# Optimization experiments

Hardware: AMD Instinct MI355X
Metric: run time of the kernel (lower is better)

Reference implementation:

```python
import jax, jax.numpy as jnp
import numpy as np

B, S, D, H = 2, 2048, 1024, 16
DK = D // H  # 64
THETA = 10000.0


def _rope_tables(seq_len, d_k, theta):
    pos = jnp.arange(seq_len, dtype=jnp.float32)  # [S]
    dim = jnp.arange(0, d_k, 2, dtype=jnp.float32)  # [DK/2]
    inv_freq = 1.0 / theta ** (dim / d_k)
    angle = pos[:, None] * inv_freq[None, :]  # [S, DK/2]
    angle = jnp.repeat(angle, 2, axis=-1)  # repeat_interleave -> [S, DK]
    return jnp.cos(angle), jnp.sin(angle)


def _apply_rope(x, cos, sin):
    # x: [..., S, DK]; interleaved pair rotation
    x1 = x[..., ::2]
    x2 = x[..., 1::2]
    x_perm = jnp.stack([-x2, x1], axis=-1).reshape(x.shape)
    return x * cos + x_perm * sin


def setup_inputs() -> dict:
    key = jax.random.key(0)
    ks = jax.random.split(key, 5)
    std = np.sqrt(2.0 / (D + D)).astype(np.float32)
    return {
        "x": jax.random.normal(ks[0], (B, S, D), dtype=jnp.float32),
        "Wq": jax.random.normal(ks[1], (D, D), dtype=jnp.float32) * std,
        "Wk": jax.random.normal(ks[2], (D, D), dtype=jnp.float32) * std,
        "Wv": jax.random.normal(ks[3], (D, D), dtype=jnp.float32) * std,
        "Wo": jax.random.normal(ks[4], (D, D), dtype=jnp.float32) * std,
    }


def reference(x, Wq, Wk, Wv, Wo):
    seq_len = x.shape[-2]
    # projections: weight is [d_out, d_in], applied as x @ W^T
    def split_heads(t):
        return t.reshape(*t.shape[:-1], H, DK).swapaxes(-3, -2)  # [B, H, S, DK]

    Q = split_heads(jnp.einsum('bsd,od->bso', x, Wq))
    K = split_heads(jnp.einsum('bsd,od->bso', x, Wk))
    V = split_heads(jnp.einsum('bsd,od->bso', x, Wv))

    cos, sin = _rope_tables(seq_len, DK, THETA)  # [S, DK]
    Q = _apply_rope(Q, cos, sin)
    K = _apply_rope(K, cos, sin)

    scale = 1.0 / np.sqrt(DK).astype(np.float32)
    logits = jnp.einsum('bhnd,bhmd->bhnm', Q, K) * scale  # [B, H, S, S]
    causal = jnp.tril(jnp.ones((seq_len, seq_len), dtype=bool))
    logits = jnp.where(causal, logits, -jnp.inf)
    probs = jax.nn.softmax(logits, axis=-1)
    attn = jnp.einsum('bhnm,bhmd->bhnd', probs, V)  # [B, H, S, DK]
    attn = attn.swapaxes(-3, -2).reshape(*x.shape[:-1], D)  # [B, S, D]
    return jnp.einsum('bsd,od->bso', attn, Wo)
```

## Files before the change

### kernel.cpp

```cpp
#include <hip/hip_runtime.h>
#include <hip/hip_bf16.h>
#include <cstdint>
#include <cstddef>

#define BB 2
#define SS 2048
#define DD 1024
#define HH 16
#define DKK 64
#define MM (BB*SS)

typedef __bf16 bf16x8 __attribute__((ext_vector_type(8)));
typedef float  f32x4  __attribute__((ext_vector_type(4)));

__device__ __forceinline__ unsigned short f2bf(float f) {
    unsigned u = __float_as_uint(f);
    u += 0x7FFF + ((u >> 16) & 1);
    return (unsigned short)(u >> 16);
}

#if __has_builtin(__builtin_amdgcn_cvt_pk_bf16_f32)
typedef __bf16 bf16v2 __attribute__((ext_vector_type(2)));
__device__ __forceinline__ unsigned pk_bf16(float a, float b) {
    bf16v2 v = __builtin_amdgcn_cvt_pk_bf16_f32(a, b);
    return __builtin_bit_cast(unsigned, v);
}
#else
__device__ __forceinline__ unsigned pk_bf16(float a, float b) {
    return (unsigned)f2bf(a) | ((unsigned)f2bf(b) << 16);
}
#endif

__device__ __forceinline__ void gld_lds16(const void* g, void* l) {
    __builtin_amdgcn_global_load_lds(
        (const __attribute__((address_space(1))) unsigned int*)g,
        (__attribute__((address_space(3))) unsigned int*)l, 16, 0, 0);
}

#define WAIT_VM8() __builtin_amdgcn_s_waitcnt(0x0F78)
#define WAIT_VM4() __builtin_amdgcn_s_waitcnt(0x0F74)
#define WAIT_VM3() __builtin_amdgcn_s_waitcnt(0x0F73)
#define WAIT_VM0() __builtin_amdgcn_s_waitcnt(0x0F70)
#define BARRIER()  __builtin_amdgcn_s_barrier()

__global__ __launch_bounds__(256) void cast_all(const float* __restrict__ x,
                                                const float* __restrict__ wq,
                                                const float* __restrict__ wk,
                                                const float* __restrict__ wv,
                                                const float* __restrict__ wo,
                                                unsigned short* __restrict__ xb,
                                                unsigned short* __restrict__ wb) {
    int i = (blockIdx.x * 256 + threadIdx.x) * 4;
    const float* src;
    unsigned short* dst;
    if (i < MM * DD) { src = x + i; dst = xb + i; }
    else {
        int e = i - MM * DD;
        int r = e >> 20;
        const float* s0 = (r == 0) ? wq : (r == 1) ? wk : (r == 2) ? wv : wo;
        src = s0 + (e & ((1 << 20) - 1));
        dst = wb + e;
    }
    float4 v = *reinterpret_cast<const float4*>(src);
    ushort4 o;
    o.x = f2bf(v.x); o.y = f2bf(v.y); o.z = f2bf(v.z); o.w = f2bf(v.w);
    *reinterpret_cast<ushort4*>(dst) = o;
}

__global__ __launch_bounds__(256, 3) void gemm_qkv(const unsigned short* __restrict__ A,
                                                   const unsigned short* __restrict__ W,
                                                   unsigned short* __restrict__ Qo,
                                                   unsigned short* __restrict__ Ko,
                                                   unsigned short* __restrict__ Vto) {
    __shared__ __align__(16) unsigned short A0[128 * 32], W0[128 * 32];
    __shared__ __align__(16) unsigned short A1[128 * 32], W1[128 * 32];
    const int tid  = threadIdx.x;
    const int wave = tid >> 6, lane = tid & 63;
    const int quad = lane >> 4, l16 = lane & 15;
    const int wm = wave >> 1, wn = wave & 1;
    const int m0 = blockIdx.y * 128, n0 = blockIdx.x * 128;
    const int sw3 = l16 & 3;

    f32x4 acc[4][4];
    for (int i = 0; i < 4; i++)
        for (int j = 0; j < 4; j++) acc[i][j] = f32x4{0.f, 0.f, 0.f, 0.f};

    auto stage = [&](int k0, unsigned short* As, unsigned short* Ws) {
        for (int c = tid; c < 512; c += 256) {
            int row = c >> 2, g = c & 3;
            int gc = ((g ^ (row & 3)) << 3);
            gld_lds16(A + (size_t)(m0 + row) * DD + k0 + gc, As + c * 8);
            gld_lds16(W + (size_t)(n0 + row) * DD + k0 + gc, Ws + c * 8);
        }
    };
    auto compute = [&](const unsigned short* As, const unsigned short* Ws) {
        bf16x8 af[4], bfb[4];
        for (int i = 0; i < 4; i++)
            af[i] = *reinterpret_cast<const bf16x8*>(As + (wm * 64 + i * 16 + l16) * 32 + ((quad ^ sw3) << 3));
        for (int j = 0; j < 4; j++)
            bfb[j] = *reinterpret_cast<const bf16x8*>(Ws + (wn * 64 + j * 16 + l16) * 32 + ((quad ^ sw3) << 3));
        for (int i = 0; i < 4; i++)
            for (int j = 0; j < 4; j++)
                acc[i][j] = __builtin_amdgcn_mfma_f32_16x16x32_bf16(af[i], bfb[j], acc[i][j], 0, 0, 0);
    };

    stage(0, A0, W0);
    int k0 = 0;
    while (true) {
        BARRIER();
        if (k0 + 32 < DD) { stage(k0 + 32, A1, W1); WAIT_VM4(); } else WAIT_VM0();
        BARRIER();
        compute(A0, W0);
        k0 += 32; if (k0 >= DD) break;

        BARRIER();
        if (k0 + 32 < DD) { stage(k0 + 32, A0, W0); WAIT_VM4(); } else WAIT_VM0();
        BARRIER();
        compute(A1, W1);
        k0 += 32; if (k0 >= DD) break;
    }

    const int region = n0 >> 10;
    const float L2T_OVER_DK = 13.287712379549449f / 64.0f;
    if (region < 2) {
        unsigned short* Co = region ? Ko : Qo;
        const float osc = (region == 0) ? 0.18033688011112042f : 1.0f;
        for (int i = 0; i < 4; i++) {
            int mrow = m0 + wm * 64 + i * 16 + quad * 4;
            int b = mrow >> 11, s0 = mrow & 2047;
            for (int j = 0; j < 4; j++) {
                int nc = (n0 + wn * 64 + j * 16 + l16) & 1023;
                int h = nc >> 6, dk = nc & 63;
                float inv_freq = exp2f(-(float)(dk & ~1) * L2T_OVER_DK);
                for (int r = 0; r < 4; r++) {
                    float v = acc[i][j][r];
                    float partner = __shfl_xor(v, 1, 64);
                    float sn, cs;
                    __sincosf((float)(s0 + r) * inv_freq, &sn, &cs);
                    float outv = (v * cs + ((dk & 1) ? partner : -partner) * sn) * osc;
                    Co[((size_t)(b * HH + h) * SS + (s0 + r)) * DKK + dk] = f2bf(outv);
                }
            }
        }
    } else {
        __syncthreads();
        unsigned short* T = A0 + wave * 1024;
        const int dkl = lane >> 2, s4 = (lane & 3) * 4;
        for (int i = 0; i < 4; i++) {
            int ms0 = m0 + wm * 64 + i * 16;
            for (int j = 0; j < 4; j++) {
                int nc0 = n0 + wn * 64 + j * 16;
                for (int r = 0; r < 4; r++)
                    T[(quad * 4 + r) * 17 + l16] = f2bf(acc[i][j][r]);
                ushort4 o;
                o.x = T[(s4 + 0) * 17 + dkl];
                o.y = T[(s4 + 1) * 17 + dkl];
                o.z = T[(s4 + 2) * 17 + dkl];
                o.w = T[(s4 + 3) * 17 + dkl];
                int nc = (nc0 + dkl) & 1023;
                int h = nc >> 6, dk = nc & 63;
                int m = ms0 + s4;
                int b = m >> 11, s = m & 2047;
                *reinterpret_cast<ushort4*>(Vto + ((size_t)((b * HH + h) * DKK + dk)) * SS + s) = o;
            }
        }
    }
}

__global__ __launch_bounds__(256, 3) void gemm_out(const unsigned short* __restrict__ A,
                                                   const unsigned short* __restrict__ W,
                                                   float* __restrict__ C) {
    __shared__ __align__(16) unsigned short A0[64 * 32], W0[128 * 32];
    __shared__ __align__(16) unsigned short A1[64 * 32], W1[128 * 32];
    const int tid  = threadIdx.x;
    const int wave = tid >> 6, lane = tid & 63;
    const int quad = lane >> 4, l16 = lane & 15;
    const int wm = wave >> 1, wn = wave & 1;
    const int m0 = blockIdx.y * 64, n0 = blockIdx.x * 128;
    const int sw3 = l16 & 3;

    f32x4 acc[2][4];
    for (int i = 0; i < 2; i++)
        for (int j = 0; j < 4; j++) acc[i][j] = f32x4{0.f, 0.f, 0.f, 0.f};

    auto stage = [&](int k0, unsigned short* As, unsigned short* Ws) {
        {
            int row = tid >> 2, g = tid & 3;
            int gc = ((g ^ (row & 3)) << 3);
            gld_lds16(A + (size_t)(m0 + row) * DD + k0 + gc, As + tid * 8);
        }
        for (int c = tid; c < 512; c += 256) {
            int row = c >> 2, g = c & 3;
            int gc = ((g ^ (row & 3)) << 3);
            gld_lds16(W + (size_t)(n0 + row) * DD + k0 + gc, Ws + c * 8);
        }
    };
    auto compute = [&](const unsigned short* As, const unsigned short* Ws) {
        bf16x8 af[2], bfb[4];
        for (int i = 0; i < 2; i++)
            af[i] = *reinterpret_cast<const bf16x8*>(As + (wm * 32 + i * 16 + l16) * 32 + ((quad ^ sw3) << 3));
        for (int j = 0; j < 4; j++)
            bfb[j] = *reinterpret_cast<const bf16x8*>(Ws + (wn * 64 + j * 16 + l16) * 32 + ((quad ^ sw3) << 3));
        for (int i = 0; i < 2; i++)
            for (int j = 0; j < 4; j++)
                acc[i][j] = __builtin_amdgcn_mfma_f32_16x16x32_bf16(af[i], bfb[j], acc[i][j], 0, 0, 0);
    };

    stage(0, A0, W0);
    int k0 = 0;
    while (true) {
        BARRIER();
        if (k0 + 32 < DD) { stage(k0 + 32, A1, W1); WAIT_VM3(); } else WAIT_VM0();
        BARRIER();
        compute(A0, W0);
        k0 += 32; if (k0 >= DD) break;

        BARRIER();
        if (k0 + 32 < DD) { stage(k0 + 32, A0, W0); WAIT_VM3(); } else WAIT_VM0();
        BARRIER();
        compute(A1, W1);
        k0 += 32; if (k0 >= DD) break;
    }

    for (int i = 0; i < 2; i++) {
        int mrow = m0 + wm * 32 + i * 16 + quad * 4;
        for (int j = 0; j < 4; j++) {
            int ncol = n0 + wn * 64 + j * 16 + l16;
            for (int r = 0; r < 4; r++)
                C[(size_t)(mrow + r) * DD + ncol] = acc[i][j][r];
        }
    }
}

__global__ __launch_bounds__(256, 3) void attn_kernel(const unsigned short* __restrict__ Qb,
                                                      const unsigned short* __restrict__ Kb,
                                                      const unsigned short* __restrict__ Vtb,
                                                      unsigned short* __restrict__ attn) {
    __shared__ unsigned short K0s[64 * 64], V0s[64 * 64];
    __shared__ unsigned short K1s[64 * 64], V1s[64 * 64];
    __shared__ unsigned short Ps[4][16 * 72];

    const int tid  = threadIdx.x;
    const int wave = tid >> 6, lane = tid & 63;
    const int quad = lane >> 4, l16 = lane & 15;

    const int lin = blockIdx.x;
    const int xcd = lin & 7, idx = lin >> 3;
    const int bh  = xcd * 4 + (idx & 3);
    const int tau = 31 - (idx >> 2);
    const int nST = tau + 1;

    const int swK = l16 & 7;
    const int q0r = tau * 64;

    const unsigned short* Qg = Qb  + (size_t)bh * SS * DKK;
    const unsigned short* Kg = Kb  + (size_t)bh * SS * DKK;
    const unsigned short* Vg = Vtb + (size_t)bh * DKK * SS;

    bf16x8 q0 = *reinterpret_cast<const bf16x8*>(Qg + (size_t)(q0r + wave * 16 + l16) * DKK + quad * 8);
    bf16x8 q1 = *reinterpret_cast<const bf16x8*>(Qg + (size_t)(q0r + wave * 16 + l16) * DKK + 32 + quad * 8);

    bf16x8 vone;
    for (int tt = 0; tt < 8; tt++) vone[tt] = (__bf16)1.0f;

    f32x4 ao[4], al;
    for (int j = 0; j < 4; j++) ao[j] = f32x4{0.f,0.f,0.f,0.f};
    al = f32x4{0.f,0.f,0.f,0.f};

    auto stage = [&](int s, unsigned short* Kd, unsigned short* Vd) {
        const int kv0 = s * 64;
        for (int c = tid; c < 512; c += 256) {
            int rowK = c >> 3, gK = c & 7;
            gld_lds16(Kg + (size_t)(kv0 + rowK) * DKK + ((gK ^ (rowK & 7)) << 3), Kd + c * 8);
            int rowV = c >> 3, gV = c & 7;
            gld_lds16(Vg + (size_t)rowV * SS + kv0 + ((gV ^ (rowV & 7)) << 3), Vd + c * 8);
        }
    };

    auto do_tile = [&](const unsigned short* Kd, const unsigned short* Vd, bool diag) {
        f32x4 sc[4];
        __builtin_amdgcn_s_setprio(1);
        for (int j = 0; j < 4; j++) {
            const unsigned short* kr = Kd + (j * 16 + l16) * 64;
            bf16x8 kf0 = *reinterpret_cast<const bf16x8*>(kr + ((quad ^ swK) << 3));
            bf16x8 kf1 = *reinterpret_cast<const bf16x8*>(kr + (((4 + quad) ^ swK) << 3));
            f32x4 s = f32x4{0.f, 0.f, 0.f, 0.f};
            s = __builtin_amdgcn_mfma_f32_16x16x32_bf16(q0, kf0, s, 0, 0, 0);
            s = __builtin_amdgcn_mfma_f32_16x16x32_bf16(q1, kf1, s, 0, 0, 0);
            sc[j] = s;
        }
        __builtin_amdgcn_s_setprio(0);
        if (diag) {
            for (int j = 0; j < 4; j++) {
                int lcol = j * 16 + l16;
                for (int r = 0; r < 4; r++) {
                    int lrow = wave * 16 + quad * 4 + r;
                    if (lcol > lrow) sc[j][r] = -1e30f;
                }
            }
        }
        for (int j = 0; j < 4; j++)
            for (int r = 0; r < 4; r++)
                sc[j][r] = exp2f(sc[j][r]);

        unsigned short* Pw = Ps[wave];
        for (int r = 0; r < 4; r++) {
            unsigned pA = pk_bf16(sc[0][r], sc[1][r]);
            unsigned pB = pk_bf16(sc[2][r], sc[3][r]);
            int ro = (quad * 4 + r) * 72;
            Pw[ro + l16]      = (unsigned short)pA;
            Pw[ro + 16 + l16] = (unsigned short)(pA >> 16);
            Pw[ro + 32 + l16] = (unsigned short)pB;
            Pw[ro + 48 + l16] = (unsigned short)(pB >> 16);
        }

        __builtin_amdgcn_s_setprio(1);
        for (int ko = 0; ko < 64; ko += 32) {
            bf16x8 pf = *reinterpret_cast<const bf16x8*>(Pw + l16 * 72 + ko + quad * 8);
            al = __builtin_amdgcn_mfma_f32_16x16x32_bf16(pf, vone, al, 0, 0, 0);
            int gg = (ko >> 3) + quad;
            for (int j = 0; j < 4; j++) {
                bf16x8 vf = *reinterpret_cast<const bf16x8*>(Vd + (j * 16 + l16) * 64 + ((gg ^ (l16 & 7)) << 3));
                ao[j] = __builtin_amdgcn_mfma_f32_16x16x32_bf16(pf, vf, ao[j], 0, 0, 0);
            }
        }
        __builtin_amdgcn_s_setprio(0);
    };

    stage(0, K0s, V0s);
    int s = 0;
    while (true) {
        BARRIER();
        if (s + 1 < nST) { stage(s + 1, K1s, V1s); WAIT_VM4(); } else WAIT_VM0();
        BARRIER();
        do_tile(K0s, V0s, s == tau);
        if (++s >= nST) break;

        BARRIER();
        if (s + 1 < nST) { stage(s + 1, K0s, V0s); WAIT_VM4(); } else WAIT_VM0();
        BARRIER();
        do_tile(K1s, V1s, s == tau);
        if (++s >= nST) break;
    }

    const int b = bh >> 4, h = bh & 15;
    for (int r = 0; r < 4; r++) {
        float invL = __builtin_amdgcn_rcpf(al[r]);
        int sr = q0r + wave * 16 + quad * 4 + r;
        for (int j = 0; j < 4; j++)
            attn[((size_t)(b * SS + sr)) * DD + h * DKK + j * 16 + l16] = f2bf(ao[j][r] * invL);
    }
}

extern "C" void kernel_launch(void* const* d_in, const int* in_sizes, int n_in,
                              void* d_out, int out_size, void* d_ws, size_t ws_size,
                              hipStream_t stream) {
    const float* x  = (const float*)d_in[0];
    const float* Wq = (const float*)d_in[1];
    const float* Wk = (const float*)d_in[2];
    const float* Wv = (const float*)d_in[3];
    const float* Wo = (const float*)d_in[4];

    char* ws = (char*)d_ws;
    const size_t MB = 1u << 20;
    unsigned short* xb    = (unsigned short*)(ws);
    unsigned short* wb    = (unsigned short*)(ws + 8  * MB);
    unsigned short* Qbuf  = (unsigned short*)(ws + 16 * MB);
    unsigned short* Kbuf  = (unsigned short*)(ws + 24 * MB);
    unsigned short* Vtbuf = (unsigned short*)(ws + 32 * MB);
    unsigned short* attnb = xb;

    cast_all<<<8192, 256, 0, stream>>>(x, Wq, Wk, Wv, Wo, xb, wb);

    gemm_qkv<<<dim3(24, 32), 256, 0, stream>>>(xb, wb, Qbuf, Kbuf, Vtbuf);

    attn_kernel<<<dim3(1024), 256, 0, stream>>>(Qbuf, Kbuf, Vtbuf, attnb);

    gemm_out<<<dim3(8, 64), 256, 0, stream>>>(attnb, wb + 3 * 1024 * 1024, (float*)d_out);
}
```

Measured before the change: 178.7 us.

## Double query rows per attention block to reuse K/V tiles across 32-row wave groups

Each attention block now covers 128 query rows (32 per wave, as two 16-row groups) instead of 64, so every K/V tile staged in shared memory feeds twice as many MFMAs. The grid shrinks to 512 blocks, diagonal tiles carry a column offset for the causal mask, and tiles lying entirely above a wave's rows are skipped. The setprio hints are also dropped. In exchange, per-wave register and LDS use rises, there are fewer blocks to balance the causal triangle, and waves in a block can have uneven work on diagonal tiles.

```diff
diff --git a/kernel.cpp b/kernel.cpp
--- a/kernel.cpp
+++ b/kernel.cpp
@@ -238,7 +238,7 @@
                                                       unsigned short* __restrict__ attn) {
     __shared__ unsigned short K0s[64 * 64], V0s[64 * 64];
     __shared__ unsigned short K1s[64 * 64], V1s[64 * 64];
-    __shared__ unsigned short Ps[4][16 * 72];
+    __shared__ unsigned short Ps[4][32 * 72];
 
     const int tid  = threadIdx.x;
     const int wave = tid >> 6, lane = tid & 63;
@@ -247,25 +247,31 @@
     const int lin = blockIdx.x;
     const int xcd = lin & 7, idx = lin >> 3;
     const int bh  = xcd * 4 + (idx & 3);
-    const int tau = 31 - (idx >> 2);
-    const int nST = tau + 1;
+    const int tau = 15 - (idx >> 2);
+    const int nST = 2 * tau + 2;
 
     const int swK = l16 & 7;
-    const int q0r = tau * 64;
+    const int q0r = tau * 128;
+    const int wq0 = wave * 32;
 
     const unsigned short* Qg = Qb  + (size_t)bh * SS * DKK;
     const unsigned short* Kg = Kb  + (size_t)bh * SS * DKK;
     const unsigned short* Vg = Vtb + (size_t)bh * DKK * SS;
 
-    bf16x8 q0 = *reinterpret_cast<const bf16x8*>(Qg + (size_t)(q0r + wave * 16 + l16) * DKK + quad * 8);
-    bf16x8 q1 = *reinterpret_cast<const bf16x8*>(Qg + (size_t)(q0r + wave * 16 + l16) * DKK + 32 + quad * 8);
+    bf16x8 qf[2][2];
+    for (int g = 0; g < 2; g++)
+        for (int h = 0; h < 2; h++)
+            qf[g][h] = *reinterpret_cast<const bf16x8*>(
+                Qg + (size_t)(q0r + wq0 + g * 16 + l16) * DKK + h * 32 + quad * 8);
 
     bf16x8 vone;
     for (int tt = 0; tt < 8; tt++) vone[tt] = (__bf16)1.0f;
 
-    f32x4 ao[4], al;
-    for (int j = 0; j < 4; j++) ao[j] = f32x4{0.f,0.f,0.f,0.f};
-    al = f32x4{0.f,0.f,0.f,0.f};
+    f32x4 ao[2][4], al[2];
+    for (int g = 0; g < 2; g++) {
+        for (int j = 0; j < 4; j++) ao[g][j] = f32x4{0.f,0.f,0.f,0.f};
+        al[g] = f32x4{0.f,0.f,0.f,0.f};
+    }
 
     auto stage = [&](int s, unsigned short* Kd, unsigned short* Vd) {
         const int kv0 = s * 64;
@@ -277,54 +283,67 @@
         }
     };
 
-    auto do_tile = [&](const unsigned short* Kd, const unsigned short* Vd, bool diag) {
-        f32x4 sc[4];
-        __builtin_amdgcn_s_setprio(1);
+    auto do_tile = [&](const unsigned short* Kd, const unsigned short* Vd,
+                       bool diag, int doff) {
+        f32x4 sc[2][4];
         for (int j = 0; j < 4; j++) {
             const unsigned short* kr = Kd + (j * 16 + l16) * 64;
             bf16x8 kf0 = *reinterpret_cast<const bf16x8*>(kr + ((quad ^ swK) << 3));
             bf16x8 kf1 = *reinterpret_cast<const bf16x8*>(kr + (((4 + quad) ^ swK) << 3));
-            f32x4 s = f32x4{0.f, 0.f, 0.f, 0.f};
-            s = __builtin_amdgcn_mfma_f32_16x16x32_bf16(q0, kf0, s, 0, 0, 0);
-            s = __builtin_amdgcn_mfma_f32_16x16x32_bf16(q1, kf1, s, 0, 0, 0);
-            sc[j] = s;
-        }
-        __builtin_amdgcn_s_setprio(0);
+            for (int g = 0; g < 2; g++) {
+                f32x4 s = f32x4{0.f, 0.f, 0.f, 0.f};
+                s = __builtin_amdgcn_mfma_f32_16x16x32_bf16(qf[g][0], kf0, s, 0, 0, 0);
+                s = __builtin_amdgcn_mfma_f32_16x16x32_bf16(qf[g][1], kf1, s, 0, 0, 0);
+                sc[g][j] = s;
+            }
+        }
         if (diag) {
-            for (int j = 0; j < 4; j++) {
-                int lcol = j * 16 + l16;
-                for (int r = 0; r < 4; r++) {
-                    int lrow = wave * 16 + quad * 4 + r;
-                    if (lcol > lrow) sc[j][r] = -1e30f;
+            for (int g = 0; g < 2; g++)
+                for (int j = 0; j < 4; j++) {
+                    int lcol = doff + j * 16 + l16;
+                    for (int r = 0; r < 4; r++) {
+                        int lrow = wq0 + g * 16 + quad * 4 + r;
+                        if (lcol > lrow) sc[g][j][r] = -1e30f;
+                    }
                 }
-            }
-        }
-        for (int j = 0; j < 4; j++)
-            for (int r = 0; r < 4; r++)
-                sc[j][r] = exp2f(sc[j][r]);
+        }
+        for (int g = 0; g < 2; g++)
+            for (int j = 0; j < 4; j++)
+                for (int r = 0; r < 4; r++)
+                    sc[g][j][r] = exp2f(sc[g][j][r]);
 
         unsigned short* Pw = Ps[wave];
-        for (int r = 0; r < 4; r++) {
-            unsigned pA = pk_bf16(sc[0][r], sc[1][r]);
-            unsigned pB = pk_bf16(sc[2][r], sc[3][r]);
-            int ro = (quad * 4 + r) * 72;
-            Pw[ro + l16]      = (unsigned short)pA;
-            Pw[ro + 16 + l16] = (unsigned short)(pA >> 16);
-            Pw[ro + 32 + l16] = (unsigned short)pB;
-            Pw[ro + 48 + l16] = (unsigned short)(pB >> 16);
-        }
-
-        __builtin_amdgcn_s_setprio(1);
+        for (int g = 0; g < 2; g++)
+            for (int r = 0; r < 4; r++) {
+                unsigned pA = pk_bf16(sc[g][0][r], sc[g][1][r]);
+                unsigned pB = pk_bf16(sc[g][2][r], sc[g][3][r]);
+                int ro = (g * 16 + quad * 4 + r) * 72;
+                Pw[ro + l16]      = (unsigned short)pA;
+                Pw[ro + 16 + l16] = (unsigned short)(pA >> 16);
+                Pw[ro + 32 + l16] = (unsigned short)pB;
+                Pw[ro + 48 + l16] = (unsigned short)(pB >> 16);
+            }
+
         for (int ko = 0; ko < 64; ko += 32) {
-            bf16x8 pf = *reinterpret_cast<const bf16x8*>(Pw + l16 * 72 + ko + quad * 8);
-            al = __builtin_amdgcn_mfma_f32_16x16x32_bf16(pf, vone, al, 0, 0, 0);
+            bf16x8 pf[2];
+            for (int g = 0; g < 2; g++) {
+                pf[g] = *reinterpret_cast<const bf16x8*>(Pw + (g * 16 + l16) * 72 + ko + quad * 8);
+                al[g] = __builtin_amdgcn_mfma_f32_16x16x32_bf16(pf[g], vone, al[g], 0, 0, 0);
+            }
             int gg = (ko >> 3) + quad;
             for (int j = 0; j < 4; j++) {
                 bf16x8 vf = *reinterpret_cast<const bf16x8*>(Vd + (j * 16 + l16) * 64 + ((gg ^ (l16 & 7)) << 3));
-                ao[j] = __builtin_amdgcn_mfma_f32_16x16x32_bf16(pf, vf, ao[j], 0, 0, 0);
-            }
-        }
-        __builtin_amdgcn_s_setprio(0);
+                for (int g = 0; g < 2; g++)
+                    ao[g][j] = __builtin_amdgcn_mfma_f32_16x16x32_bf16(pf[g], vf, ao[g][j], 0, 0, 0);
+            }
+        }
+    };
+
+    auto step = [&](const unsigned short* Kd, const unsigned short* Vd, int s) {
+        bool diag = (s >= 2 * tau);
+        int doff = (s - 2 * tau) * 64;
+        if (!diag) do_tile(Kd, Vd, false, 0);
+        else if (doff <= wq0 + 31) do_tile(Kd, Vd, true, doff);
     };
 
     stage(0, K0s, V0s);
@@ -333,23 +352,24 @@
         BARRIER();
         if (s + 1 < nST) { stage(s + 1, K1s, V1s); WAIT_VM4(); } else WAIT_VM0();
         BARRIER();
-        do_tile(K0s, V0s, s == tau);
+        step(K0s, V0s, s);
         if (++s >= nST) break;
 
         BARRIER();
         if (s + 1 < nST) { stage(s + 1, K0s, V0s); WAIT_VM4(); } else WAIT_VM0();
         BARRIER();
-        do_tile(K1s, V1s, s == tau);
+        step(K1s, V1s, s);
         if (++s >= nST) break;
     }
 
     const int b = bh >> 4, h = bh & 15;
-    for (int r = 0; r < 4; r++) {
-        float invL = __builtin_amdgcn_rcpf(al[r]);
-        int sr = q0r + wave * 16 + quad * 4 + r;
-        for (int j = 0; j < 4; j++)
-            attn[((size_t)(b * SS + sr)) * DD + h * DKK + j * 16 + l16] = f2bf(ao[j][r] * invL);
-    }
+    for (int g = 0; g < 2; g++)
+        for (int r = 0; r < 4; r++) {
+            float invL = __builtin_amdgcn_rcpf(al[g][r]);
+            int sr = q0r + wq0 + g * 16 + quad * 4 + r;
+            for (int j = 0; j < 4; j++)
+                attn[((size_t)(b * SS + sr)) * DD + h * DKK + j * 16 + l16] = f2bf(ao[g][j][r] * invL);
+        }
 }
 
 extern "C" void kernel_launch(void* const* d_in, const int* in_sizes, int n_in,
@@ -374,7 +394,7 @@
 
     gemm_qkv<<<dim3(24, 32), 256, 0, stream>>>(xb, wb, Qbuf, Kbuf, Vtbuf);
 
-    attn_kernel<<<dim3(1024), 256, 0, stream>>>(Qbuf, Kbuf, Vtbuf, attnb);
+    attn_kernel<<<dim3(512), 256, 0, stream>>>(Qbuf, Kbuf, Vtbuf, attnb);
 
     gemm_out<<<dim3(8, 64), 256, 0, stream>>>(attnb, wb + 3 * 1024 * 1024, (float*)d_out);
 }
```

After: 193.6 us. 1.08x slower.
